# Optimization experiments

Hardware: AMD Instinct MI355X
Metric: run time of the kernel (lower is better)

The kernel has to match this reference:

```python
import jax, jax.numpy as jnp
import numpy as np

NBITS = 4
QN = -2 ** (NBITS - 1)          # -8
QP = 2 ** (NBITS - 1) - 1       # 7
POT = list(range(QN, QP + 1))   # additive_pot = [-8..7]


def hadamard_matrix(n):
    # Sylvester construction, normalized (orthonormal rotation).
    H = np.array([[1.0]], dtype=np.float32)
    while H.shape[0] < n:
        H = np.block([[H, H], [H, -H]])
    return (H / np.sqrt(n)).astype(np.float32)


def grad_scale(x, scale):
    y_grad = x * scale
    return jax.lax.stop_gradient(x - y_grad) + y_grad


def round_ste(x):
    return x + jax.lax.stop_gradient(jnp.round(x) - x)


def act_quant(x, alpha, beta):
    # Act_Quant.forward, trained/eval state with signed==1.
    x = x + beta
    g = 1.0 / np.sqrt(x.size * QP)
    a = grad_scale(alpha, g)
    q = round_ste(jnp.clip(x / a, QN, QP))
    return q * a - beta


def round_ltq(x, a_pos):
    # oneRK_U.round_ltq: learnable-threshold quantizer with STE-style backward.
    x_forward = jnp.full_like(x, float(POT[0]))
    slope0 = (POT[1] - POT[0]) / (a_pos[1] - a_pos[0])
    y0 = slope0 * x + POT[0] - slope0 * a_pos[0]
    x_backward = jnp.where(x > a_pos[0], y0, 0.1 * x + POT[0] - 0.1 * a_pos[0])
    n = len(POT)
    for i in range(1, n):
        thre_f = (a_pos[i - 1] + a_pos[i]) / 2
        if i != n - 1:
            slope = (POT[i + 1] - POT[i]) / (a_pos[i + 1] - a_pos[i])
            y_step = slope * x + POT[i] - slope * a_pos[i]
        else:
            y_step = x
        x_forward = jnp.where(x > thre_f, float(POT[i]), x_forward)
        x_backward = jnp.where(x > a_pos[i], y_step, x_backward)
    x_backward = jnp.where(x > a_pos[n - 1], 0.1 * x + POT[n - 1] - 0.1 * a_pos[n - 1], x_backward)
    return jax.lax.stop_gradient(x_forward) + x_backward - jax.lax.stop_gradient(x_backward)


def weight_quant(w, alpha, beta, a_pos):
    # oneRK_U.forward, trained/eval state with signed==1.
    w = w + beta
    g = 1.0 / np.sqrt(w.size * QP)
    a = grad_scale(alpha, g)
    q = round_ltq(jnp.clip(w / a, QN, QP), a_pos)
    return q * a - beta


def setup_inputs() -> dict:
    key = jax.random.key(0)
    k1, k2, k3 = jax.random.split(key, 3)
    B, S, D_IN, D_OUT = 4, 2048, 4096, 4096
    H = hadamard_matrix(D_IN)
    x = jax.random.normal(k1, (B, S, D_IN), dtype=jnp.float32)
    # Had_linear.__init__ rotates the stored weight: weight <- had(weight)
    w_raw = jax.random.normal(k2, (D_OUT, D_IN), dtype=jnp.float32) * 0.02
    weight = w_raw @ jnp.asarray(H)
    bias = jax.random.normal(k3, (D_OUT,), dtype=jnp.float32) * 0.01
    return {
        "x": x,
        "weight": weight,
        "bias": bias,
        "alpha_a": jnp.array([0.6], dtype=jnp.float32),   # ~ 2*E|x|/sqrt(Qp)
        "beta_a": jnp.zeros((1,), dtype=jnp.float32),
        "alpha_w": jnp.array([0.012], dtype=jnp.float32),  # ~ 2*E|w|/sqrt(Qp)
        "beta_w": jnp.zeros((1,), dtype=jnp.float32),
        "a_w": jnp.arange(QN, QP + 1, dtype=jnp.float32),  # trained a = [-8..7]
    }


def reference(x, weight, bias, alpha_a, beta_a, alpha_w, beta_w, a_w):
    D_IN = x.shape[-1]
    H = jnp.asarray(hadamard_matrix(D_IN))
    xr = x @ H                                   # Hadamard rotation [B,S,D]
    x_q = act_quant(xr, alpha_a, beta_a)         # fake-quant activations
    w_q = weight_quant(weight, alpha_w, beta_w, a_w)  # fake-quant weights
    return jnp.einsum('bsd,od->bso', x_q, w_q) + bias
```

## Files before the change

### kernel.cpp

```cpp
#include <hip/hip_runtime.h>
#include <hip/hip_bf16.h>
#include <stdint.h>

typedef int    i32x4 __attribute__((ext_vector_type(4)));
typedef unsigned char u8;

#define HD 4096

#define PAD(i) ((i) + (((i) >> 6) << 2))

#define FWHT16(v) do { \
  _Pragma("unroll") \
  for (int st = 0; st < 4; ++st) { \
    const int sg = 1 << st; \
    _Pragma("unroll") \
    for (int g = 0; g < 16; g += 2 * sg) { \
      _Pragma("unroll") \
      for (int k2 = 0; k2 < sg; ++k2) { \
        float ua = v[g + k2], ub = v[g + k2 + sg]; \
        v[g + k2] = ua + ub; \
        v[g + k2 + sg] = ua - ub; \
      } \
    } \
  } \
} while (0)

__global__ __launch_bounds__(256) void fwht_actq(
    const float* __restrict__ x, const float* __restrict__ alpha,
    const float* __restrict__ beta, u8* __restrict__ qx,
    float* __restrict__ Sx)
{
  __shared__ float s[PAD(4095) + 1];
  const int row = blockIdx.x;
  const int t = threadIdx.x;
  const float* xin = x + (size_t)row * HD;
  float v[16];

  #pragma unroll
  for (int j = 0; j < 16; ++j) v[j] = xin[t + 256 * j];
  FWHT16(v);
  #pragma unroll
  for (int j = 0; j < 16; ++j) { int i0 = t + 256 * j; s[PAD(i0)] = v[j]; }
  __syncthreads();

  const int bb = t & 15, cc = t >> 4;
  #pragma unroll
  for (int j = 0; j < 16; ++j) { int i0 = bb + 16 * j + 256 * cc; v[j] = s[PAD(i0)]; }
  FWHT16(v);
  #pragma unroll
  for (int j = 0; j < 16; ++j) { int i0 = bb + 16 * j + 256 * cc; s[PAD(i0)] = v[j]; }
  __syncthreads();

  {
    const float4* p4 = (const float4*)&s[16 * t + ((t >> 2) << 2)];
    #pragma unroll
    for (int q = 0; q < 4; ++q) {
      float4 f = p4[q];
      v[q * 4 + 0] = f.x; v[q * 4 + 1] = f.y; v[q * 4 + 2] = f.z; v[q * 4 + 3] = f.w;
    }
  }
  FWHT16(v);

  const float al = alpha[0];
  const float be = beta[0];
  float qsum = 0.f;
  int pk[4];
  #pragma unroll
  for (int c4 = 0; c4 < 4; ++c4) {
    int w32 = 0;
    #pragma unroll
    for (int k = 0; k < 4; ++k) {
      float xv = v[c4 * 4 + k] * 0.015625f + be;
      float tq = xv / al;
      tq = fminf(fmaxf(tq, -8.f), 7.f);
      float qq = rintf(tq);
      qsum += qq;
      w32 |= ((int)qq & 0xFF) << (k * 8);
    }
    pk[c4] = w32;
  }
  *(int4*)(qx + (size_t)row * HD + 16 * t) = make_int4(pk[0], pk[1], pk[2], pk[3]);

  __syncthreads();
  s[t] = qsum;
  __syncthreads();
  for (int o = 128; o > 0; o >>= 1) {
    if (t < o) s[t] += s[t + o];
    __syncthreads();
  }
  if (t == 0) Sx[row] = s[0];
}

__global__ __launch_bounds__(256) void wq_kernel(
    const float* __restrict__ w, const float* __restrict__ alpha,
    const float* __restrict__ beta, const float* __restrict__ a_w,
    u8* __restrict__ qw, float* __restrict__ Sw)
{
  __shared__ float red[256];
  const int row = blockIdx.x;
  const int t = threadIdx.x;
  const float al = alpha[0];
  const float be = beta[0];
  float th[15];
  #pragma unroll
  for (int i = 0; i < 15; ++i) th[i] = 0.5f * (a_w[i] + a_w[i + 1]);

  float qsum = 0.f;
  int* qw32 = (int*)(qw + (size_t)row * HD);
  #pragma unroll
  for (int c = 0; c < 4; ++c) {
    int e = c * 1024 + t * 4;
    float4 v = *(const float4*)(w + (size_t)row * HD + e);
    float vv[4] = {v.x, v.y, v.z, v.w};
    int pk = 0;
    #pragma unroll
    for (int k = 0; k < 4; ++k) {
      float xv = vv[k] + be;
      float tq = xv / al;
      tq = fminf(fmaxf(tq, -8.f), 7.f);
      float qq = -8.f;
      #pragma unroll
      for (int i = 0; i < 15; ++i) qq = (tq > th[i]) ? (float)(i - 7) : qq;
      qsum += qq;
      pk |= ((int)qq & 0xFF) << (k * 8);
    }
    qw32[c * 256 + t] = pk;
  }

  red[t] = qsum;
  __syncthreads();
  for (int o = 128; o > 0; o >>= 1) {
    if (t < o) red[t] += red[t + o];
    __syncthreads();
  }
  if (t == 0) Sw[row] = red[0];
}

#define LDS_BOFF 65536

__device__ __forceinline__ void gload_lds16(const void* g, void* l) {
  __builtin_amdgcn_global_load_lds(
      (__attribute__((address_space(1))) void*)((void*)g),
      (__attribute__((address_space(3))) void*)(l), 16, 0, 0);
}

#define STAGE_A(buf, u, kh) do { \
  gload_lds16(gA0 + (size_t)(u) * 128 + (kh) * 64, &lds[(buf)*32768 + (kh)*16384 + wv*1024]); \
  gload_lds16(gA1 + (size_t)(u) * 128 + (kh) * 64, &lds[(buf)*32768 + (kh)*16384 + 8192 + wv*1024]); \
} while (0)

#define STAGE_B(buf, u, kh) do { \
  gload_lds16(gB0 + (size_t)(u) * 128 + (kh) * 64, &lds[LDS_BOFF + (buf)*32768 + (kh)*16384 + wv*1024]); \
  gload_lds16(gB1 + (size_t)(u) * 128 + (kh) * 64, &lds[LDS_BOFF + (buf)*32768 + (kh)*16384 + 8192 + wv*1024]); \
} while (0)

#define CPWAIT(n) asm volatile("s_waitcnt vmcnt(" #n ")" ::: "memory")
#define NOSTMT ((void)0)

#define PHASE(p, kk, ch, STAGE_STMT, CP_STMT) do { \
  if ((ch) == 0) { \
    _Pragma("unroll") \
    for (int n = 0; n < 4; ++n) \
      b[n] = *(const i32x4*)&lds[LDS_BOFF + (p)*32768 + (kk)*16384 + posB[n]]; \
  } \
  _Pragma("unroll") \
  for (int i = 0; i < 4; ++i) \
    a[i] = *(const i32x4*)&lds[(p)*32768 + (kk)*16384 + posA[(ch)*4 + i]]; \
  STAGE_STMT; \
  __builtin_amdgcn_sched_barrier(0); \
  __builtin_amdgcn_s_barrier(); \
  asm volatile("s_waitcnt lgkmcnt(0)" ::: "memory"); \
  __builtin_amdgcn_sched_barrier(0); \
  __builtin_amdgcn_s_setprio(1); \
  _Pragma("unroll") \
  for (int i = 0; i < 4; ++i) { \
    _Pragma("unroll") \
    for (int n = 0; n < 4; ++n) \
      acc[(ch)*4 + i][n] = __builtin_amdgcn_mfma_i32_16x16x64_i8(a[i], b[n], acc[(ch)*4 + i][n], 0, 0, 0); \
  } \
  __builtin_amdgcn_s_setprio(0); \
  __builtin_amdgcn_sched_barrier(0); \
  CP_STMT; \
  __builtin_amdgcn_s_barrier(); \
  __builtin_amdgcn_sched_barrier(0); \
} while (0)

#define TILEBODY(p, t) do { \
  PHASE(p, 0, 0, STAGE_A(1-(p), (t)+1, 0), NOSTMT); \
  PHASE(p, 0, 1, STAGE_B(1-(p), (t)+1, 0), CPWAIT(4)); \
  PHASE(p, 1, 0, STAGE_A(1-(p), (t)+1, 1), NOSTMT); \
  PHASE(p, 1, 1, STAGE_B(1-(p), (t)+1, 1), CPWAIT(4)); \
} while (0)

#define TILELAST(p) do { \
  PHASE(p, 0, 0, NOSTMT, NOSTMT); \
  PHASE(p, 0, 1, NOSTMT, CPWAIT(0)); \
  PHASE(p, 1, 0, NOSTMT, NOSTMT); \
  PHASE(p, 1, 1, NOSTMT, NOSTMT); \
} while (0)

__global__ __launch_bounds__(512, 2) void gemm_qq(
    const u8* __restrict__ qx, const u8* __restrict__ qw,
    const float* __restrict__ bias, const float* __restrict__ Sx,
    const float* __restrict__ Sw,
    const float* __restrict__ p_aa, const float* __restrict__ p_ba,
    const float* __restrict__ p_aw, const float* __restrict__ p_bw,
    float* __restrict__ out, int M, int N, int K)
{
  __shared__ u8 lds[131072];
  const int tid  = threadIdx.x;
  const int lane = tid & 63;
  const int wv   = tid >> 6;
  const int wm   = wv >> 2;
  const int wn   = wv & 3;

  const int bid  = blockIdx.x;
  const int wgid = (bid & 7) * 64 + (bid >> 3);
  const int bm   = wgid >> 4;
  const int bn   = wgid & 15;

  int posA[8], posB[4];
  #pragma unroll
  for (int fm = 0; fm < 8; ++fm) {
    int row = wm * 128 + fm * 16 + (lane & 15);
    posA[fm] = (((row >> 3) * 32) + (lane >> 4) * 8 + (row & 7)) * 16;
  }
  #pragma unroll
  for (int n = 0; n < 4; ++n) {
    int col = wn * 64 + n * 16 + (lane & 15);
    posB[n] = (((col >> 3) * 32) + (lane >> 4) * 8 + (col & 7)) * 16;
  }

  const int rs0 = (tid >> 5) * 8 + (tid & 7);
  const int rs1 = 128 + rs0;
  const int kcs = ((tid >> 3) & 3) * 16;
  const u8* gA0 = qx + (size_t)(bm * 256 + rs0) * K + kcs;
  const u8* gA1 = qx + (size_t)(bm * 256 + rs1) * K + kcs;
  const u8* gB0 = qw + (size_t)(bn * 256 + rs0) * K + kcs;
  const u8* gB1 = qw + (size_t)(bn * 256 + rs1) * K + kcs;

  i32x4 acc[8][4] = {};
  i32x4 a[4], b[4];

  STAGE_A(0, 0, 0);
  STAGE_B(0, 0, 0);
  STAGE_A(0, 0, 1);
  STAGE_B(0, 0, 1);
  CPWAIT(4);
  __builtin_amdgcn_sched_barrier(0);
  __builtin_amdgcn_s_barrier();
  __builtin_amdgcn_sched_barrier(0);

  for (int t = 0; t < 30; t += 2) {
    TILEBODY(0, t);
    TILEBODY(1, t + 1);
  }
  TILEBODY(0, 30);
  TILELAST(1);

  const float aa = p_aa[0], ba = p_ba[0], aw = p_aw[0], bw = p_bw[0];
  const float scale  = aa * aw;
  const float rowmul = -aa * bw;
  const float colmul = -aw * ba;
  const float cterm  = (float)K * ba * bw;

  #pragma unroll
  for (int n = 0; n < 4; ++n) {
    const int col = bn * 256 + wn * 64 + n * 16 + (lane & 15);
    const float colc = bias[col] + colmul * Sw[col] + cterm;
    #pragma unroll
    for (int fm = 0; fm < 8; ++fm) {
      const int row0 = bm * 256 + wm * 128 + fm * 16 + ((lane >> 4) << 2);
      #pragma unroll
      for (int j2 = 0; j2 < 4; ++j2) {
        const int row = row0 + j2;
        out[(size_t)row * N + col] = (float)acc[fm][n][j2] * scale + rowmul * Sx[row] + colc;
      }
    }
  }
}

extern "C" void kernel_launch(void* const* d_in, const int* in_sizes, int n_in,
                              void* d_out, int out_size, void* d_ws, size_t ws_size,
                              hipStream_t stream) {
  const float* x       = (const float*)d_in[0];
  const float* wgt     = (const float*)d_in[1];
  const float* bias    = (const float*)d_in[2];
  const float* alpha_a = (const float*)d_in[3];
  const float* beta_a  = (const float*)d_in[4];
  const float* alpha_w = (const float*)d_in[5];
  const float* beta_w  = (const float*)d_in[6];
  const float* a_w     = (const float*)d_in[7];

  const int K = HD;
  const int M = in_sizes[0] / K;
  const int N = in_sizes[1] / K;

  char* ws = (char*)d_ws;
  u8* qx = (u8*)ws;
  u8* qw = (u8*)(ws + (size_t)M * K);
  float* Sx = (float*)(ws + (size_t)M * K + (size_t)N * K);
  float* Sw = Sx + M;

  fwht_actq<<<M, 256, 0, stream>>>(x, alpha_a, beta_a, qx, Sx);
  wq_kernel<<<N, 256, 0, stream>>>(wgt, alpha_w, beta_w, a_w, qw, Sw);

  const int nwg = (N / 256) * (M / 256);
  gemm_qq<<<nwg, 512, 0, stream>>>(qx, qw, bias, Sx, Sw,
                                   alpha_a, beta_a, alpha_w, beta_w,
                                   (float*)d_out, M, N, K);
}
```

Measured before the change: 215.7 us.

## Restructure int8 GEMM main loop into two phases per K tile

Replaces the four-phase-per-tile schedule with two phases. Each phase now loads both K halves of A and B fragments and issues 32 MFMAs, which halves the number of workgroup barriers per tile. All next-tile global-to-LDS prefetches are issued in the first phase and waited on with vmcnt(0) at the end of the second. This doubles the fragment registers held (a[8], b[8]), which adds register pressure under launch_bounds(512,2). It also gives less fine-grained overlap of the copy waits.

```diff
diff --git a/kernel.cpp b/kernel.cpp
--- a/kernel.cpp
+++ b/kernel.cpp
@@ -154,18 +154,29 @@
   gload_lds16(gB1 + (size_t)(u) * 128 + (kh) * 64, &lds[LDS_BOFF + (buf)*32768 + (kh)*16384 + 8192 + wv*1024]); \
 } while (0)
 
+#define STAGE_ALL(buf, u) do { \
+  STAGE_A(buf, u, 0); \
+  STAGE_A(buf, u, 1); \
+  STAGE_B(buf, u, 0); \
+  STAGE_B(buf, u, 1); \
+} while (0)
+
 #define CPWAIT(n) asm volatile("s_waitcnt vmcnt(" #n ")" ::: "memory")
 #define NOSTMT ((void)0)
 
-#define PHASE(p, kk, ch, STAGE_STMT, CP_STMT) do { \
-  if ((ch) == 0) { \
-    _Pragma("unroll") \
-    for (int n = 0; n < 4; ++n) \
-      b[n] = *(const i32x4*)&lds[LDS_BOFF + (p)*32768 + (kk)*16384 + posB[n]]; \
-  } \
+#define PHASE0(p, STAGE_STMT) do { \
+  _Pragma("unroll") \
+  for (int n = 0; n < 4; ++n) \
+    b[n] = *(const i32x4*)&lds[LDS_BOFF + (p)*32768 + posB[n]]; \
+  _Pragma("unroll") \
+  for (int n = 0; n < 4; ++n) \
+    b[4 + n] = *(const i32x4*)&lds[LDS_BOFF + (p)*32768 + 16384 + posB[n]]; \
   _Pragma("unroll") \
   for (int i = 0; i < 4; ++i) \
-    a[i] = *(const i32x4*)&lds[(p)*32768 + (kk)*16384 + posA[(ch)*4 + i]]; \
+    a[i] = *(const i32x4*)&lds[(p)*32768 + posA[i]]; \
+  _Pragma("unroll") \
+  for (int i = 0; i < 4; ++i) \
+    a[4 + i] = *(const i32x4*)&lds[(p)*32768 + 16384 + posA[i]]; \
   STAGE_STMT; \
   __builtin_amdgcn_sched_barrier(0); \
   __builtin_amdgcn_s_barrier(); \
@@ -176,7 +187,43 @@
   for (int i = 0; i < 4; ++i) { \
     _Pragma("unroll") \
     for (int n = 0; n < 4; ++n) \
-      acc[(ch)*4 + i][n] = __builtin_amdgcn_mfma_i32_16x16x64_i8(a[i], b[n], acc[(ch)*4 + i][n], 0, 0, 0); \
+      acc[i][n] = __builtin_amdgcn_mfma_i32_16x16x64_i8(a[i], b[n], acc[i][n], 0, 0, 0); \
+  } \
+  _Pragma("unroll") \
+  for (int i = 0; i < 4; ++i) { \
+    _Pragma("unroll") \
+    for (int n = 0; n < 4; ++n) \
+      acc[i][n] = __builtin_amdgcn_mfma_i32_16x16x64_i8(a[4 + i], b[4 + n], acc[i][n], 0, 0, 0); \
+  } \
+  __builtin_amdgcn_s_setprio(0); \
+  __builtin_amdgcn_sched_barrier(0); \
+  __builtin_amdgcn_s_barrier(); \
+  __builtin_amdgcn_sched_barrier(0); \
+} while (0)
+
+#define PHASE1(p, CP_STMT) do { \
+  _Pragma("unroll") \
+  for (int i = 0; i < 4; ++i) \
+    a[i] = *(const i32x4*)&lds[(p)*32768 + posA[4 + i]]; \
+  _Pragma("unroll") \
+  for (int i = 0; i < 4; ++i) \
+    a[4 + i] = *(const i32x4*)&lds[(p)*32768 + 16384 + posA[4 + i]]; \
+  __builtin_amdgcn_sched_barrier(0); \
+  __builtin_amdgcn_s_barrier(); \
+  asm volatile("s_waitcnt lgkmcnt(0)" ::: "memory"); \
+  __builtin_amdgcn_sched_barrier(0); \
+  __builtin_amdgcn_s_setprio(1); \
+  _Pragma("unroll") \
+  for (int i = 0; i < 4; ++i) { \
+    _Pragma("unroll") \
+    for (int n = 0; n < 4; ++n) \
+      acc[4 + i][n] = __builtin_amdgcn_mfma_i32_16x16x64_i8(a[i], b[n], acc[4 + i][n], 0, 0, 0); \
+  } \
+  _Pragma("unroll") \
+  for (int i = 0; i < 4; ++i) { \
+    _Pragma("unroll") \
+    for (int n = 0; n < 4; ++n) \
+      acc[4 + i][n] = __builtin_amdgcn_mfma_i32_16x16x64_i8(a[4 + i], b[4 + n], acc[4 + i][n], 0, 0, 0); \
   } \
   __builtin_amdgcn_s_setprio(0); \
   __builtin_amdgcn_sched_barrier(0); \
@@ -186,17 +233,13 @@
 } while (0)
 
 #define TILEBODY(p, t) do { \
-  PHASE(p, 0, 0, STAGE_A(1-(p), (t)+1, 0), NOSTMT); \
-  PHASE(p, 0, 1, STAGE_B(1-(p), (t)+1, 0), CPWAIT(4)); \
-  PHASE(p, 1, 0, STAGE_A(1-(p), (t)+1, 1), NOSTMT); \
-  PHASE(p, 1, 1, STAGE_B(1-(p), (t)+1, 1), CPWAIT(4)); \
+  PHASE0(p, STAGE_ALL(1-(p), (t)+1)); \
+  PHASE1(p, CPWAIT(0)); \
 } while (0)
 
 #define TILELAST(p) do { \
-  PHASE(p, 0, 0, NOSTMT, NOSTMT); \
-  PHASE(p, 0, 1, NOSTMT, CPWAIT(0)); \
-  PHASE(p, 1, 0, NOSTMT, NOSTMT); \
-  PHASE(p, 1, 1, NOSTMT, NOSTMT); \
+  PHASE0(p, NOSTMT); \
+  PHASE1(p, NOSTMT); \
 } while (0)
 
 __global__ __launch_bounds__(512, 2) void gemm_qq(
@@ -240,13 +283,10 @@
   const u8* gB1 = qw + (size_t)(bn * 256 + rs1) * K + kcs;
 
   i32x4 acc[8][4] = {};
-  i32x4 a[4], b[4];
-
-  STAGE_A(0, 0, 0);
-  STAGE_B(0, 0, 0);
-  STAGE_A(0, 0, 1);
-  STAGE_B(0, 0, 1);
-  CPWAIT(4);
+  i32x4 a[8], b[8];
+
+  STAGE_ALL(0, 0);
+  CPWAIT(0);
   __builtin_amdgcn_sched_barrier(0);
   __builtin_amdgcn_s_barrier();
   __builtin_amdgcn_sched_barrier(0);
```

New measurement: 239.0 us. 1.11x slower.

## Double-buffer LDS fragment registers to overlap reads with MFMA

Applied to the files above, without the earlier changes.

The int8 GEMM main loop now keeps two register sets for A and B fragments and issues LDS reads for the next phase right after the barrier, so they run while the current phase's MFMAs execute instead of before them. The global-load wait counts are tightened so the prefetch of the next tile's first fragments sees completed data. This adds 32 more VGPRs of fragment storage, which may pressure occupancy at 2 blocks of 512 threads, and makes the vmcnt and barrier ordering more delicate.

```diff
diff --git a/kernel.cpp b/kernel.cpp
--- a/kernel.cpp
+++ b/kernel.cpp
@@ -157,46 +157,52 @@
 #define CPWAIT(n) asm volatile("s_waitcnt vmcnt(" #n ")" ::: "memory")
 #define NOSTMT ((void)0)
 
-#define PHASE(p, kk, ch, STAGE_STMT, CP_STMT) do { \
-  if ((ch) == 0) { \
-    _Pragma("unroll") \
-    for (int n = 0; n < 4; ++n) \
-      b[n] = *(const i32x4*)&lds[LDS_BOFF + (p)*32768 + (kk)*16384 + posB[n]]; \
-  } \
+#define PRE_A(dst, p, kh, ch) do { \
   _Pragma("unroll") \
   for (int i = 0; i < 4; ++i) \
-    a[i] = *(const i32x4*)&lds[(p)*32768 + (kk)*16384 + posA[(ch)*4 + i]]; \
+    dst[i] = *(const i32x4*)&lds[(p)*32768 + (kh)*16384 + posA[(ch)*4 + i]]; \
+} while (0)
+
+#define PRE_B(dst, p, kh) do { \
+  _Pragma("unroll") \
+  for (int n = 0; n < 4; ++n) \
+    dst[n] = *(const i32x4*)&lds[LDS_BOFF + (p)*32768 + (kh)*16384 + posB[n]]; \
+} while (0)
+
+#define PHASEX(STAGE_STMT, ACC0, ASET, BSET, PRE_STMT, CP_STMT) do { \
   STAGE_STMT; \
   __builtin_amdgcn_sched_barrier(0); \
   __builtin_amdgcn_s_barrier(); \
   asm volatile("s_waitcnt lgkmcnt(0)" ::: "memory"); \
   __builtin_amdgcn_sched_barrier(0); \
+  PRE_STMT; \
   __builtin_amdgcn_s_setprio(1); \
   _Pragma("unroll") \
   for (int i = 0; i < 4; ++i) { \
     _Pragma("unroll") \
     for (int n = 0; n < 4; ++n) \
-      acc[(ch)*4 + i][n] = __builtin_amdgcn_mfma_i32_16x16x64_i8(a[i], b[n], acc[(ch)*4 + i][n], 0, 0, 0); \
+      acc[(ACC0) + i][n] = __builtin_amdgcn_mfma_i32_16x16x64_i8(ASET[i], BSET[n], acc[(ACC0) + i][n], 0, 0, 0); \
   } \
   __builtin_amdgcn_s_setprio(0); \
   __builtin_amdgcn_sched_barrier(0); \
   CP_STMT; \
+  __builtin_amdgcn_sched_barrier(0); \
   __builtin_amdgcn_s_barrier(); \
   __builtin_amdgcn_sched_barrier(0); \
 } while (0)
 
 #define TILEBODY(p, t) do { \
-  PHASE(p, 0, 0, STAGE_A(1-(p), (t)+1, 0), NOSTMT); \
-  PHASE(p, 0, 1, STAGE_B(1-(p), (t)+1, 0), CPWAIT(4)); \
-  PHASE(p, 1, 0, STAGE_A(1-(p), (t)+1, 1), NOSTMT); \
-  PHASE(p, 1, 1, STAGE_B(1-(p), (t)+1, 1), CPWAIT(4)); \
+  PHASEX(STAGE_A(1-(p), (t)+1, 0), 0, a0, b0, PRE_A(a1, p, 0, 1), CPWAIT(2)); \
+  PHASEX(STAGE_B(1-(p), (t)+1, 0), 4, a1, b0, { PRE_B(b1, p, 1); PRE_A(a0, p, 1, 0); }, NOSTMT); \
+  PHASEX(STAGE_A(1-(p), (t)+1, 1), 0, a0, b1, PRE_A(a1, p, 1, 1), CPWAIT(2)); \
+  PHASEX(STAGE_B(1-(p), (t)+1, 1), 4, a1, b1, { PRE_B(b0, 1-(p), 0); PRE_A(a0, 1-(p), 0, 0); }, NOSTMT); \
 } while (0)
 
 #define TILELAST(p) do { \
-  PHASE(p, 0, 0, NOSTMT, NOSTMT); \
-  PHASE(p, 0, 1, NOSTMT, CPWAIT(0)); \
-  PHASE(p, 1, 0, NOSTMT, NOSTMT); \
-  PHASE(p, 1, 1, NOSTMT, NOSTMT); \
+  PHASEX(NOSTMT, 0, a0, b0, PRE_A(a1, p, 0, 1), CPWAIT(0)); \
+  PHASEX(NOSTMT, 4, a1, b0, { PRE_B(b1, p, 1); PRE_A(a0, p, 1, 0); }, NOSTMT); \
+  PHASEX(NOSTMT, 0, a0, b1, PRE_A(a1, p, 1, 1), NOSTMT); \
+  PHASEX(NOSTMT, 4, a1, b1, NOSTMT, NOSTMT); \
 } while (0)
 
 __global__ __launch_bounds__(512, 2) void gemm_qq(
@@ -240,7 +246,7 @@
   const u8* gB1 = qw + (size_t)(bn * 256 + rs1) * K + kcs;
 
   i32x4 acc[8][4] = {};
-  i32x4 a[4], b[4];
+  i32x4 a0[4], a1[4], b0[4], b1[4];
 
   STAGE_A(0, 0, 0);
   STAGE_B(0, 0, 0);
@@ -250,6 +256,8 @@
   __builtin_amdgcn_sched_barrier(0);
   __builtin_amdgcn_s_barrier();
   __builtin_amdgcn_sched_barrier(0);
+  PRE_B(b0, 0, 0);
+  PRE_A(a0, 0, 0, 0);
 
   for (int t = 0; t < 30; t += 2) {
     TILEBODY(0, t);
```

Measured after the change: 221.3 us. +2.6%, slower.
